# Kernel tuning notes

Measured on AMD Instinct MI355X. Metric: run time of the kernel, lower is better.

Reference implementation:

```python
import jax, jax.numpy as jnp
import numpy as np

N_HEAD = 16

def setup_inputs() -> dict:
    key = jax.random.key(0)
    ks = jax.random.split(key, 5)
    C = 1024
    s = 0.02
    return {
        "x": jax.random.normal(ks[0], (4, 2048, C), dtype=jnp.float32),
        "w_attn": jax.random.normal(ks[1], (C, 3 * C), dtype=jnp.float32) * s,
        "b_attn": jnp.zeros((3 * C,), dtype=jnp.float32),
        "w_proj": jax.random.normal(ks[2], (C, C), dtype=jnp.float32) * s,
        "b_proj": jnp.zeros((C,), dtype=jnp.float32),
    }

def reference(x, w_attn, b_attn, w_proj, b_proj):
    B, T, C = x.shape
    H = N_HEAD
    D = C // H
    qkv = x @ w_attn + b_attn                      # [B,T,3C]
    q, k, v = jnp.split(qkv, 3, axis=-1)
    # [B,H,T,D]
    q = q.reshape(B, T, H, D).transpose(0, 2, 1, 3)
    k = k.reshape(B, T, H, D).transpose(0, 2, 1, 3)
    v = v.reshape(B, T, H, D).transpose(0, 2, 1, 3)
    scale = 1.0 / np.sqrt(D).astype(np.float32)
    attn = jnp.einsum('bhtd,bhsd->bhts', q, k) * scale   # [B,H,T,T]
    causal = jnp.tril(jnp.ones((T, T), dtype=bool))
    attn = jnp.where(causal, attn, -jnp.inf)
    attn = jax.nn.softmax(attn, axis=-1)
    y = jnp.einsum('bhts,bhsd->bhtd', attn, v)           # [B,H,T,D]
    y = y.transpose(0, 2, 1, 3).reshape(B, T, C)
    return y @ w_proj + b_proj
```

## Files before the change

kernel.cpp:

```cpp
#include <hip/hip_runtime.h>
#include <hip/hip_bf16.h>

typedef short short8 __attribute__((ext_vector_type(8)));
typedef float f32x4 __attribute__((ext_vector_type(4)));
typedef float f32x16 __attribute__((ext_vector_type(16)));

typedef __attribute__((address_space(1))) void as1_void;
typedef __attribute__((address_space(3))) void as3_void;

__device__ __forceinline__ unsigned short f2bf(float f) {
    __hip_bfloat16 h = __float2bfloat16(f);
    return __builtin_bit_cast(unsigned short, h);
}

__device__ __forceinline__ float exp2fast(float x) {
    return __builtin_amdgcn_exp2f(x);
}

__device__ __forceinline__ unsigned int cvtpk(float lo, float hi) {
    unsigned int r;
    asm("v_cvt_pk_bf16_f32 %0, %1, %2" : "=v"(r) : "v"(lo), "v"(hi));
    return r;
}

__device__ __forceinline__ void plswap(unsigned int& a, unsigned int& b) {
    asm("v_permlane32_swap_b32 %0, %1" : "+v"(a), "+v"(b));
}

__device__ __forceinline__ void gload16(const unsigned short* g, unsigned short* l) {
    __builtin_amdgcn_global_load_lds((as1_void*)g, (as3_void*)l, 16, 0, 0);
}

__global__ __launch_bounds__(256) void conv_f32_to_bf16(
    const float* __restrict__ in, unsigned short* __restrict__ out, int n4) {
    int i = blockIdx.x * 256 + threadIdx.x;
    if (i >= n4) return;
    float4 v = ((const float4*)in)[i];
    ushort4 o;
    o.x = f2bf(v.x); o.y = f2bf(v.y); o.z = f2bf(v.z); o.w = f2bf(v.w);
    ((ushort4*)out)[i] = o;
}

__global__ __launch_bounds__(256) void transpose_f32_to_bf16(
    const float* __restrict__ W, unsigned short* __restrict__ WT, int K, int N) {
    __shared__ float tile[32][33];
    int tx = threadIdx.x, ty = threadIdx.y;
    int n0 = blockIdx.x * 32, k0 = blockIdx.y * 32;
#pragma unroll
    for (int j = 0; j < 4; ++j)
        tile[ty + j * 8][tx] = W[(size_t)(k0 + ty + j * 8) * N + n0 + tx];
    __syncthreads();
#pragma unroll
    for (int j = 0; j < 4; ++j)
        WT[(size_t)(n0 + ty + j * 8) * K + k0 + tx] = f2bf(tile[tx][ty + j * 8]);
}

template <int MODE>
__global__ __launch_bounds__(256, 2) void gemm_bt(
    const unsigned short* __restrict__ A,
    const unsigned short* __restrict__ Bt,
    const float* __restrict__ bias,
    void* __restrict__ out0,
    unsigned short* __restrict__ out1,
    int M, int N, int K) {
    __shared__ unsigned short sA[128 * 64];
    __shared__ unsigned short sB[128 * 64];
    const int tid = threadIdx.x;
    const int lane = tid & 63;
    const int w = tid >> 6;
    const int wr = (w >> 1) * 64;
    const int wc = (w & 1) * 64;
    const size_t arow0 = (size_t)blockIdx.x * 128;
    const size_t brow0 = (size_t)blockIdx.y * 128;

    const int grow = (w << 5) + (lane >> 3);
    const int gcolswz = (((lane & 7) ^ ((lane >> 3) & 7)) << 3);
    const unsigned short* pA0 = A + (arow0 + grow) * (size_t)K + gcolswz;
    const unsigned short* pB0 = Bt + (brow0 + grow) * (size_t)K + gcolswz;
    unsigned short* lA = sA + (w << 11);
    unsigned short* lB = sB + (w << 11);

    f32x4 acc[4][4] = {};
    const int fr = lane & 15;
    const int g = lane >> 4;

    for (int k0 = 0; k0 < K; k0 += 64) {
        __syncthreads();
#pragma unroll
        for (int j = 0; j < 4; ++j) {
            gload16(pA0 + (size_t)(j * 8) * K + k0, lA + j * 512);
            gload16(pB0 + (size_t)(j * 8) * K + k0, lB + j * 512);
        }
        __syncthreads();

#pragma unroll
        for (int kc = 0; kc < 2; ++kc) {
            short8 af[4], bfr[4];
#pragma unroll
            for (int i = 0; i < 4; ++i) {
                const int row = wr + i * 16 + fr;
                af[i] = *(const short8*)&sA[row * 64 +
                                            (((kc * 4 + g) ^ (row & 7)) << 3)];
            }
#pragma unroll
            for (int i = 0; i < 4; ++i) {
                const int row = wc + i * 16 + fr;
                bfr[i] = *(const short8*)&sB[row * 64 +
                                             (((kc * 4 + g) ^ (row & 7)) << 3)];
            }
#pragma unroll
            for (int mi = 0; mi < 4; ++mi)
#pragma unroll
                for (int ni = 0; ni < 4; ++ni)
                    acc[mi][ni] = __builtin_amdgcn_mfma_f32_16x16x32_bf16(
                        af[mi], bfr[ni], acc[mi][ni], 0, 0, 0);
        }
    }

    const int fq = (lane >> 4) << 2;
    if constexpr (MODE == 0) {
#pragma unroll
        for (int mi = 0; mi < 4; ++mi)
#pragma unroll
            for (int ni = 0; ni < 4; ++ni) {
                size_t r = arow0 + wr + mi * 16 + fq;
                size_t c = brow0 + wc + ni * 16 + fr;
                float bv = bias[c];
#pragma unroll
                for (int j = 0; j < 4; ++j)
                    ((float*)out0)[(r + j) * (size_t)N + c] = acc[mi][ni][j] + bv;
            }
    } else {
        const bool isv = (int)(brow0 + wc) >= 2048;
        if (isv) {
#pragma unroll
            for (int mi = 0; mi < 4; ++mi)
#pragma unroll
                for (int ni = 0; ni < 4; ++ni) {
                    int c = (int)brow0 + wc + ni * 16 + fr;
                    float bv = bias[c];
                    int cv = c - 2048;
                    int r0 = (int)arow0 + wr + mi * 16 + fq;
                    int bb = r0 >> 11, t0 = r0 & 2047;
                    unsigned int lo = (unsigned int)f2bf(acc[mi][ni][0] + bv) |
                                      ((unsigned int)f2bf(acc[mi][ni][1] + bv) << 16);
                    unsigned int hi = (unsigned int)f2bf(acc[mi][ni][2] + bv) |
                                      ((unsigned int)f2bf(acc[mi][ni][3] + bv) << 16);
                    *(uint2*)&out1[(((size_t)(bb * 1024 + cv)) << 11) + t0] =
                        make_uint2(lo, hi);
                }
        } else {
            const float qs = ((int)(brow0 + wc) < 1024) ? 0.125f * 1.4426950408889634f
                                                        : 1.0f;
#pragma unroll
            for (int mi = 0; mi < 4; ++mi)
#pragma unroll
                for (int ni = 0; ni < 4; ++ni) {
                    size_t r = arow0 + wr + mi * 16 + fq;
                    size_t c = brow0 + wc + ni * 16 + fr;
                    float bv = bias[c];
#pragma unroll
                    for (int j = 0; j < 4; ++j)
                        ((unsigned short*)out0)[(r + j) * 2048 + c] =
                            f2bf((acc[mi][ni][j] + bv) * qs);
                }
        }
    }
}

__global__ __launch_bounds__(256, 3) void attn_mfma(
    const unsigned short* __restrict__ qk,
    const unsigned short* __restrict__ vt,
    unsigned short* __restrict__ y,
    int BH) {
    constexpr int T = 2048;
    constexpr float THR = 8.0f;

    __shared__ __align__(16) unsigned short sK[2][64 * 64];
    __shared__ __align__(16) unsigned short sV[2][64 * 64];

    const int tid = threadIdx.x;
    const int lane = tid & 63;
    const int w = tid >> 6;
    const int l31 = lane & 31;
    const int b5 = lane >> 5;

    const int bh = blockIdx.x % BH;
    const int qt = 15 - blockIdx.x / BH;
    const int b = bh >> 4;
    const int h = bh & 15;
    const int q0 = qt << 7;
    const int qw0 = q0 + w * 32;

    const unsigned short* kbase = qk + ((size_t)(b * T)) * 2048 + 1024 + h * 64;
    const unsigned short* vbase = vt + ((size_t)(b * 1024 + h * 64)) * 2048;

    const int srow = tid >> 3;
    const int c16 = tid & 7;
    const int swz = ((c16 ^ (srow & 7)) << 3);

    short8 vones;
#pragma unroll
    for (int i = 0; i < 8; ++i) vones[i] = (short)0x3F80;

    short8 aq[4];
    {
        const unsigned short* qbase =
            qk + ((size_t)(b * T + qw0 + l31)) * 2048 + h * 64;
#pragma unroll
        for (int kc = 0; kc < 4; ++kc)
            aq[kc] = *(const short8*)(qbase + b5 * 8 + kc * 16);
    }

    f32x16 O0 = {}, O1 = {};
    f32x16 l_st = {};
    float m_st = -1e30f;

    const int nt = (q0 + 128) >> 6;

    uint4 kd0, kd1, vd0, vd1;
    kd0 = *(const uint4*)(kbase + (size_t)(srow) * 2048 + c16 * 8);
    kd1 = *(const uint4*)(kbase + (size_t)(srow + 32) * 2048 + c16 * 8);
    vd0 = *(const uint4*)(vbase + (size_t)srow * 2048 + c16 * 8);
    vd1 = *(const uint4*)(vbase + (size_t)(srow + 32) * 2048 + c16 * 8);
    *(uint4*)&sK[0][srow * 64 + swz] = kd0;
    *(uint4*)&sK[0][(srow + 32) * 64 + swz] = kd1;
    *(uint4*)&sV[0][srow * 64 + swz] = vd0;
    *(uint4*)&sV[0][(srow + 32) * 64 + swz] = vd1;
    __syncthreads();

    int cur = 0;
    for (int it = 0; it < nt; ++it) {
        const int s0 = it << 6;
        const bool haveNext = (it + 1 < nt);
        if (haveNext) {
            const int s1 = s0 + 64;
            kd0 = *(const uint4*)(kbase + (size_t)(s1 + srow) * 2048 + c16 * 8);
            kd1 = *(const uint4*)(kbase + (size_t)(s1 + srow + 32) * 2048 + c16 * 8);
            vd0 = *(const uint4*)(vbase + (size_t)srow * 2048 + s1 + c16 * 8);
            vd1 = *(const uint4*)(vbase + (size_t)(srow + 32) * 2048 + s1 + c16 * 8);
        }
        const unsigned short* sKc = sK[cur];
        const unsigned short* sVc = sV[cur];

        if (s0 <= qw0 + 31) {
            f32x16 sacc[2] = {};
            __builtin_amdgcn_s_setprio(1);
#pragma unroll
            for (int kc = 0; kc < 4; ++kc) {
#pragma unroll
                for (int ni = 0; ni < 2; ++ni) {
                    const int row = ni * 32 + l31;
                    short8 akf = *(const short8*)&sKc[row * 64 +
                                                      (((b5 + kc * 2) ^ (row & 7))
                                                       << 3)];
                    sacc[ni] = __builtin_amdgcn_mfma_f32_32x32x16_bf16(
                        akf, aq[kc], sacc[ni], 0, 0, 0);
                }
            }
            __builtin_amdgcn_s_setprio(0);

            const bool needMask = (s0 + 63 > qw0);
            const int qg = qw0 + l31;
            if (needMask) {
#pragma unroll
                for (int ni = 0; ni < 2; ++ni)
#pragma unroll
                    for (int reg = 0; reg < 16; ++reg) {
                        const int sg = s0 + ni * 32 + (reg & 3) + 8 * (reg >> 2) +
                                       4 * b5;
                        sacc[ni][reg] = (sg <= qg) ? sacc[ni][reg] : -INFINITY;
                    }
            }

            float mt[16];
#pragma unroll
            for (int i = 0; i < 16; ++i)
                mt[i] = fmaxf(sacc[0][i], sacc[1][i]);
#pragma unroll
            for (int st = 8; st > 0; st >>= 1)
#pragma unroll
                for (int i = 0; i < 8; ++i)
                    if (i < st) mt[i] = fmaxf(mt[i], mt[i + st]);
            float mx = mt[0];
            mx = fmaxf(mx, __shfl_xor(mx, 32));

            const bool resc = __any(mx > m_st + THR);
            float f_l = 1.0f;
            if (resc) {
                const float mn = fmaxf(m_st, mx);
                f_l = exp2fast(m_st - mn);
                m_st = mn;
            }

#pragma unroll
            for (int ni = 0; ni < 2; ++ni)
#pragma unroll
                for (int reg = 0; reg < 16; ++reg)
                    sacc[ni][reg] = exp2fast(sacc[ni][reg] - m_st);

            short8 pa[4];
#pragma unroll
            for (int c = 0; c < 4; ++c) {
                const int ni = c >> 1;
                const int off = (c & 1) * 8;
                unsigned int pk01 = cvtpk(sacc[ni][off + 0], sacc[ni][off + 1]);
                unsigned int pk23 = cvtpk(sacc[ni][off + 2], sacc[ni][off + 3]);
                unsigned int pk45 = cvtpk(sacc[ni][off + 4], sacc[ni][off + 5]);
                unsigned int pk67 = cvtpk(sacc[ni][off + 6], sacc[ni][off + 7]);
                plswap(pk01, pk45);
                plswap(pk23, pk67);
                uint4 u = make_uint4(pk01, pk23, pk45, pk67);
                pa[c] = __builtin_bit_cast(short8, u);
            }

            if (resc) {
                const int fil = __builtin_bit_cast(int, f_l);
#pragma unroll
                for (int reg = 0; reg < 16; ++reg) {
                    const int qpat = (reg & 3) + 8 * (reg >> 2) + 4 * b5;
                    const float fq = __builtin_bit_cast(
                        float, __builtin_amdgcn_ds_bpermute(
                                   (qpat + (lane & 32)) << 2, fil));
                    O0[reg] *= fq;
                    O1[reg] *= fq;
                    l_st[reg] *= fq;
                }
            }

            f32x16 lacc = {};
            __builtin_amdgcn_s_setprio(1);
#pragma unroll
            for (int c = 0; c < 4; ++c) {
                lacc = __builtin_amdgcn_mfma_f32_32x32x16_bf16(
                    pa[c], vones, lacc, 0, 0, 0);
                {
                    const int row = l31;
                    short8 bvf = *(const short8*)&sVc[row * 64 +
                                                      (((c * 2 + b5) ^ (row & 7))
                                                       << 3)];
                    O0 = __builtin_amdgcn_mfma_f32_32x32x16_bf16(
                        pa[c], bvf, O0, 0, 0, 0);
                }
                {
                    const int row = 32 + l31;
                    short8 bvf = *(const short8*)&sVc[row * 64 +
                                                      (((c * 2 + b5) ^ (row & 7))
                                                       << 3)];
                    O1 = __builtin_amdgcn_mfma_f32_32x32x16_bf16(
                        pa[c], bvf, O1, 0, 0, 0);
                }
            }
            __builtin_amdgcn_s_setprio(0);
#pragma unroll
            for (int reg = 0; reg < 16; ++reg) l_st[reg] += lacc[reg];
        }

        if (haveNext) {
            unsigned short* sKn = sK[cur ^ 1];
            unsigned short* sVn = sV[cur ^ 1];
            *(uint4*)&sKn[srow * 64 + swz] = kd0;
            *(uint4*)&sKn[(srow + 32) * 64 + swz] = kd1;
            *(uint4*)&sVn[srow * 64 + swz] = vd0;
            *(uint4*)&sVn[(srow + 32) * 64 + swz] = vd1;
        }
        __syncthreads();
        cur ^= 1;
    }

#pragma unroll
    for (int reg = 0; reg < 16; ++reg) {
        const int qpat = (reg & 3) + 8 * (reg >> 2) + 4 * b5;
        const float inv = 1.0f / l_st[reg];
        const size_t base = (size_t)(b * T + qw0 + qpat) * 1024 + h * 64 + l31;
        y[base] = f2bf(O0[reg] * inv);
        y[base + 32] = f2bf(O1[reg] * inv);
    }
}

extern "C" void kernel_launch(void* const* d_in, const int* in_sizes, int n_in,
                              void* d_out, int out_size, void* d_ws, size_t ws_size,
                              hipStream_t stream) {
    const float* x      = (const float*)d_in[0];
    const float* w_attn = (const float*)d_in[1];
    const float* b_attn = (const float*)d_in[2];
    const float* w_proj = (const float*)d_in[3];
    const float* b_proj = (const float*)d_in[4];

    const int C = 1024, T = 2048, H = 16;
    const int B = in_sizes[0] / (T * C);
    const int M = B * T;

    unsigned short* xb  = (unsigned short*)d_ws;
    unsigned short* wTa = xb + (size_t)M * C;
    unsigned short* wTp = wTa + (size_t)3 * C * C;
    unsigned short* qkb = wTp + (size_t)C * C;
    unsigned short* vtb = qkb + (size_t)M * 2 * C;
    unsigned short* y   = xb;

    int n4 = (M * C) / 4;
    conv_f32_to_bf16<<<(n4 + 255) / 256, 256, 0, stream>>>(x, xb, n4);
    transpose_f32_to_bf16<<<dim3(3 * C / 32, C / 32), dim3(32, 8), 0, stream>>>(
        w_attn, wTa, C, 3 * C);
    transpose_f32_to_bf16<<<dim3(C / 32, C / 32), dim3(32, 8), 0, stream>>>(
        w_proj, wTp, C, C);
    gemm_bt<2><<<dim3(M / 128, (3 * C) / 128), 256, 0, stream>>>(
        xb, wTa, b_attn, (void*)qkb, vtb, M, 3 * C, C);
    attn_mfma<<<dim3((B * H) * 16), 256, 0, stream>>>(qkb, vtb, y, B * H);
    gemm_bt<0><<<dim3(M / 128, C / 128), 256, 0, stream>>>(
        y, wTp, b_proj, d_out, nullptr, M, C, C);
}
```

Measured before the change: 163.8 us.

## Prefetch K two tiles ahead, fold row-sum into MFMA, merge weight transposes

The attention loop now loads K tiles two iterations ahead into alternating register sets, while V is still loaded one iteration ahead. This gives global K loads more time to complete before they are written to shared memory. The row-sum MFMA now accumulates directly into l_st instead of a temporary that was added afterwards. The two weight transpose launches are merged into one kernel that picks the matrix from the block index, saving a launch. The trade-off is more live registers, which may lower occupancy.

New measurement: 160.7 us. No clear change (-1.9%).

```diff
diff --git a/kernel.cpp b/kernel.cpp
--- a/kernel.cpp
+++ b/kernel.cpp
@@ -41,11 +41,19 @@
     ((ushort4*)out)[i] = o;
 }
 
-__global__ __launch_bounds__(256) void transpose_f32_to_bf16(
-    const float* __restrict__ W, unsigned short* __restrict__ WT, int K, int N) {
+__global__ __launch_bounds__(256) void transpose2_f32_to_bf16(
+    const float* __restrict__ Wa, const float* __restrict__ Wp,
+    unsigned short* __restrict__ WTa, unsigned short* __restrict__ WTp) {
     __shared__ float tile[32][33];
+    const int K = 1024;
+    int bx = blockIdx.x;
+    const float* W;
+    unsigned short* WT;
+    int N, n0;
+    if (bx < 96) { W = Wa; WT = WTa; N = 3072; n0 = bx * 32; }
+    else         { W = Wp; WT = WTp; N = 1024; n0 = (bx - 96) * 32; }
     int tx = threadIdx.x, ty = threadIdx.y;
-    int n0 = blockIdx.x * 32, k0 = blockIdx.y * 32;
+    int k0 = blockIdx.y * 32;
 #pragma unroll
     for (int j = 0; j < 4; ++j)
         tile[ty + j * 8][tx] = W[(size_t)(k0 + ty + j * 8) * N + n0 + tx];
@@ -218,30 +226,45 @@
 
     const int nt = (q0 + 128) >> 6;
 
-    uint4 kd0, kd1, vd0, vd1;
-    kd0 = *(const uint4*)(kbase + (size_t)(srow) * 2048 + c16 * 8);
-    kd1 = *(const uint4*)(kbase + (size_t)(srow + 32) * 2048 + c16 * 8);
+    uint4 kA0, kA1, kB0, kB1, vd0, vd1;
+    kA0 = *(const uint4*)(kbase + (size_t)(srow) * 2048 + c16 * 8);
+    kA1 = *(const uint4*)(kbase + (size_t)(srow + 32) * 2048 + c16 * 8);
     vd0 = *(const uint4*)(vbase + (size_t)srow * 2048 + c16 * 8);
     vd1 = *(const uint4*)(vbase + (size_t)(srow + 32) * 2048 + c16 * 8);
-    *(uint4*)&sK[0][srow * 64 + swz] = kd0;
-    *(uint4*)&sK[0][(srow + 32) * 64 + swz] = kd1;
+    *(uint4*)&sK[0][srow * 64 + swz] = kA0;
+    *(uint4*)&sK[0][(srow + 32) * 64 + swz] = kA1;
     *(uint4*)&sV[0][srow * 64 + swz] = vd0;
     *(uint4*)&sV[0][(srow + 32) * 64 + swz] = vd1;
+    kB0 = *(const uint4*)(kbase + (size_t)(64 + srow) * 2048 + c16 * 8);
+    kB1 = *(const uint4*)(kbase + (size_t)(64 + srow + 32) * 2048 + c16 * 8);
     __syncthreads();
 
-    int cur = 0;
     for (int it = 0; it < nt; ++it) {
         const int s0 = it << 6;
         const bool haveNext = (it + 1 < nt);
+        const bool have2 = (it + 2 < nt);
+        if (it & 1) {
+            if (have2) {
+                const int s2 = s0 + 128;
+                kB0 = *(const uint4*)(kbase + (size_t)(s2 + srow) * 2048 + c16 * 8);
+                kB1 = *(const uint4*)(kbase + (size_t)(s2 + srow + 32) * 2048 +
+                                      c16 * 8);
+            }
+        } else {
+            if (have2) {
+                const int s2 = s0 + 128;
+                kA0 = *(const uint4*)(kbase + (size_t)(s2 + srow) * 2048 + c16 * 8);
+                kA1 = *(const uint4*)(kbase + (size_t)(s2 + srow + 32) * 2048 +
+                                      c16 * 8);
+            }
+        }
         if (haveNext) {
             const int s1 = s0 + 64;
-            kd0 = *(const uint4*)(kbase + (size_t)(s1 + srow) * 2048 + c16 * 8);
-            kd1 = *(const uint4*)(kbase + (size_t)(s1 + srow + 32) * 2048 + c16 * 8);
             vd0 = *(const uint4*)(vbase + (size_t)srow * 2048 + s1 + c16 * 8);
             vd1 = *(const uint4*)(vbase + (size_t)(srow + 32) * 2048 + s1 + c16 * 8);
         }
-        const unsigned short* sKc = sK[cur];
-        const unsigned short* sVc = sV[cur];
+        const unsigned short* sKc = sK[it & 1];
+        const unsigned short* sVc = sV[it & 1];
 
         if (s0 <= qw0 + 31) {
             f32x16 sacc[2] = {};
@@ -328,12 +351,11 @@
                 }
             }
 
-            f32x16 lacc = {};
             __builtin_amdgcn_s_setprio(1);
 #pragma unroll
             for (int c = 0; c < 4; ++c) {
-                lacc = __builtin_amdgcn_mfma_f32_32x32x16_bf16(
-                    pa[c], vones, lacc, 0, 0, 0);
+                l_st = __builtin_amdgcn_mfma_f32_32x32x16_bf16(
+                    pa[c], vones, l_st, 0, 0, 0);
                 {
                     const int row = l31;
                     short8 bvf = *(const short8*)&sVc[row * 64 +
@@ -352,20 +374,22 @@
                 }
             }
             __builtin_amdgcn_s_setprio(0);
-#pragma unroll
-            for (int reg = 0; reg < 16; ++reg) l_st[reg] += lacc[reg];
         }
 
         if (haveNext) {
-            unsigned short* sKn = sK[cur ^ 1];
-            unsigned short* sVn = sV[cur ^ 1];
-            *(uint4*)&sKn[srow * 64 + swz] = kd0;
-            *(uint4*)&sKn[(srow + 32) * 64 + swz] = kd1;
+            unsigned short* sKn = sK[(it + 1) & 1];
+            unsigned short* sVn = sV[(it + 1) & 1];
+            if (it & 1) {
+                *(uint4*)&sKn[srow * 64 + swz] = kA0;
+                *(uint4*)&sKn[(srow + 32) * 64 + swz] = kA1;
+            } else {
+                *(uint4*)&sKn[srow * 64 + swz] = kB0;
+                *(uint4*)&sKn[(srow + 32) * 64 + swz] = kB1;
+            }
             *(uint4*)&sVn[srow * 64 + swz] = vd0;
             *(uint4*)&sVn[(srow + 32) * 64 + swz] = vd1;
         }
         __syncthreads();
-        cur ^= 1;
     }
 
 #pragma unroll
@@ -400,10 +424,8 @@
 
     int n4 = (M * C) / 4;
     conv_f32_to_bf16<<<(n4 + 255) / 256, 256, 0, stream>>>(x, xb, n4);
-    transpose_f32_to_bf16<<<dim3(3 * C / 32, C / 32), dim3(32, 8), 0, stream>>>(
-        w_attn, wTa, C, 3 * C);
-    transpose_f32_to_bf16<<<dim3(C / 32, C / 32), dim3(32, 8), 0, stream>>>(
-        w_proj, wTp, C, C);
+    transpose2_f32_to_bf16<<<dim3(128, 32), dim3(32, 8), 0, stream>>>(
+        w_attn, w_proj, wTa, wTp);
     gemm_bt<2><<<dim3(M / 128, (3 * C) / 128), 256, 0, stream>>>(
         xb, wTa, b_attn, (void*)qkb, vtb, M, 3 * C, C);
     attn_mfma<<<dim3((B * H) * 16), 256, 0, stream>>>(qkb, vtb, y, B * H);
```
